# Kernel optimization log

Hardware: AMD Instinct MI355X
Metric: run time of the kernel (lower is better)

## Reference

```python
import jax, jax.numpy as jnp
import numpy as np

B = 131072      # batch of states
N_ACT = 40      # output_dim (Tetris action space)


def setup_inputs() -> dict:
    key = jax.random.key(0)
    ks = jax.random.split(key, 9)
    # state vector: 11 real-valued board features, 1 hold-piece id in [0,4),
    # 3 next-piece ids in [1,8) (0 is treated as invalid by the original code)
    keep = jax.random.normal(ks[0], (B, 11), dtype=jnp.float32)
    hold = jax.random.randint(ks[1], (B, 1), 0, 4).astype(jnp.float32)
    nxt = jax.random.randint(ks[2], (B, 3), 1, 8).astype(jnp.float32)
    x = jnp.concatenate([keep, hold, nxt], axis=1)  # [B, 15]
    W1 = jax.random.normal(ks[3], (36, 128), dtype=jnp.float32) * 0.1
    b1 = jnp.zeros((128,), dtype=jnp.float32)
    W2 = jax.random.normal(ks[4], (128, 512), dtype=jnp.float32) * 0.05
    b2 = jnp.zeros((512,), dtype=jnp.float32)
    W4 = jax.random.normal(ks[5], (512, N_ACT), dtype=jnp.float32) * 0.05
    b4 = jnp.zeros((N_ACT,), dtype=jnp.float32)
    return {"x": x, "W1": W1, "b1": b1, "W2": W2, "b2": b2, "W4": W4, "b4": b4}


def reference(x, W1, b1, W2, b2, W4, b4):
    B_, _ = x.shape
    keep = x[:, :11]                                      # [B, 11]
    # vectorized replacement of the per-sample .item() one-hot loop
    hold_idx = jax.lax.stop_gradient(jnp.clip(x[:, 11].astype(jnp.int32), 0, 3))
    nxt_idx = jax.lax.stop_gradient(jnp.clip(x[:, 12:15].astype(jnp.int32) - 1, 0, 6))
    hold_oh = jax.nn.one_hot(hold_idx, 4, dtype=x.dtype)  # [B, 4]
    nxt_oh = jax.nn.one_hot(nxt_idx, 7, dtype=x.dtype).reshape(B_, 21)  # [B, 21]
    inp = jnp.concatenate([keep, hold_oh, nxt_oh], axis=1)  # [B, 36]
    h = jax.nn.relu(inp @ W1 + b1)   # [B, 128]
    h = jax.nn.relu(h @ W2 + b2)     # [B, 512]
    return h @ W4 + b4               # [B, N_ACT]
```

## Files before the change

### kernel.cpp

```cpp
#include <hip/hip_runtime.h>


typedef short bf16x8 __attribute__((ext_vector_type(8)));
typedef float f32x4 __attribute__((ext_vector_type(4)));
typedef unsigned int u32;

#define NW1F 8192
#define NW2F 65536
#define NW4F 24576
#define PACK_TOTAL (NW1F + NW2F + NW4F)
#define PACK_THREADS (PACK_TOTAL / 8)

#define SROW 72

__device__ __forceinline__ unsigned short f2bf(float f) {
  union { float f; unsigned u; } a; a.f = f;
  unsigned r = a.u + 0x7fffu + ((a.u >> 16) & 1u);
  return (unsigned short)(r >> 16);
}
__device__ __forceinline__ u32 cvtpk(float lo, float hi) {
  u32 r;
  asm("v_cvt_pk_bf16_f32 %0, %1, %2" : "=v"(r) : "v"(lo), "v"(hi));
  return r;
}

__global__ void pack_weights(const float* __restrict__ W1,
                             const float* __restrict__ W2,
                             const float* __restrict__ W4,
                             unsigned short* __restrict__ wf) {
  int t = blockIdx.x * 256 + threadIdx.x;
  if (t >= PACK_THREADS) return;
  int fid = t >> 6, lane = t & 63;
  int l16 = lane & 15, quad = lane >> 4;
  float vals[8];
  if (fid < 16) {
    int mt = fid >> 1, ks = fid & 1;
    int m = mt * 16 + l16, k0 = ks * 32 + quad * 8;
#pragma unroll
    for (int j = 0; j < 8; ++j) { int k = k0 + j; vals[j] = (k < 36) ? W1[k * 128 + m] : 0.f; }
  } else if (fid < 144) {
    int f = fid - 16, mt = f >> 2, ks = f & 3;
    int m = mt * 16 + l16, k0 = ks * 32 + quad * 8;
#pragma unroll
    for (int j = 0; j < 8; ++j) vals[j] = W2[(k0 + j) * 512 + m];
  } else {
    int f = fid - 144, mt = f >> 4, ks = f & 15;
    int m = mt * 16 + l16, k0 = ks * 32 + quad * 8;
#pragma unroll
    for (int j = 0; j < 8; ++j) vals[j] = (m < 40) ? W4[(k0 + j) * 40 + m] : 0.f;
  }
  u32 p[4];
#pragma unroll
  for (int j = 0; j < 4; ++j) p[j] = cvtpk(vals[2 * j], vals[2 * j + 1]);
  *(bf16x8*)(wf + (size_t)t * 8) = *(bf16x8*)p;
}

#define MTL_STEP(chunk, mtl)                                                   \
  {                                                                            \
    f32x4 bias2 = *(const f32x4*)(b2 + (chunk) * 64 + (mtl) * 16 + quad * 4);  \
    int fb = (chunk) * 16 + (mtl) * 4 + 4;                                     \
    if (fb >= 128) fb = 0;           \
    _Pragma("unroll")                                                          \
    for (int k = 0; k < 4; ++k)                                                \
      W[((mtl) + 1) & 1][k] = *(const bf16x8*)(w2p + (size_t)(fb + k) * 512);  \
    f32x4 acc2[2];                                                             \
    __builtin_amdgcn_s_setprio(1);                                             \
    _Pragma("unroll")                                                          \
    for (int rg = 0; rg < 2; ++rg)                                             \
      acc2[rg] = __builtin_amdgcn_mfma_f32_16x16x32_bf16(                      \
          W[(mtl) & 1][0], af1[rg][0], bias2, 0, 0, 0);                        \
    _Pragma("unroll")                                                          \
    for (int ks = 1; ks < 4; ++ks)                                             \
      _Pragma("unroll")                                                        \
      for (int rg = 0; rg < 2; ++rg)                                           \
        acc2[rg] = __builtin_amdgcn_mfma_f32_16x16x32_bf16(                    \
            W[(mtl) & 1][ks], af1[rg][ks], acc2[rg], 0, 0, 0);                 \
    __builtin_amdgcn_s_setprio(0);                                             \
    _Pragma("unroll")                                                          \
    for (int rg = 0; rg < 2; ++rg) {                                           \
      float v0 = fmaxf(acc2[rg][0], 0.f);                                      \
      float v1 = fmaxf(acc2[rg][1], 0.f);                                      \
      float v2 = fmaxf(acc2[rg][2], 0.f);                                      \
      float v3 = fmaxf(acc2[rg][3], 0.f);                                      \
      uint2 pk = {cvtpk(v0, v1), cvtpk(v2, v3)};                               \
      *(uint2*)(su + (rg * 16 + l16) * SROW + (mtl) * 16 + quad * 4) = pk;     \
    }                                                                          \
  }

#define H_READ(dst, ks3)                                                       \
  _Pragma("unroll")                                                            \
  for (int rg = 0; rg < 2; ++rg)                                               \
    dst[rg] = *(const bf16x8*)(su + (rg * 16 + l16) * SROW + (ks3) * 32 + quad * 8);

#define W4_LOAD(dst, chunkprev, ks3)                                           \
  _Pragma("unroll")                                                            \
  for (int mt3 = 0; mt3 < 3; ++mt3)                                            \
    dst[mt3] = *(const bf16x8*)(                                               \
        w4f + (size_t)((mt3 * 16 + (chunkprev) * 2 + (ks3)) * 64 + lane) * 8);

#define L3_PART(w4q, hq)                                                       \
  __builtin_amdgcn_s_setprio(1);                                               \
  _Pragma("unroll")                                                            \
  for (int mt3 = 0; mt3 < 3; ++mt3)                                            \
    _Pragma("unroll")                                                          \
    for (int rg = 0; rg < 2; ++rg)                                             \
      accO[mt3][rg] = __builtin_amdgcn_mfma_f32_16x16x32_bf16(                 \
          w4q[mt3], hq[rg], accO[mt3][rg], 0, 0, 0);                           \
  __builtin_amdgcn_s_setprio(0);

__global__ __launch_bounds__(128, 4) void dqn_fused(
    const float* __restrict__ x,
    const unsigned short* __restrict__ wf,
    const float* __restrict__ b1,
    const float* __restrict__ b2,
    const float* __restrict__ b4,
    float* __restrict__ out) {
  __shared__ __align__(16) unsigned short sBuf[2 * 32 * SROW];

  const int tid  = threadIdx.x;
  const int lane = tid & 63;
  const int wave = tid >> 6;
  const int quad = lane >> 4;
  const int l16  = lane & 15;
  const int row0 = blockIdx.x << 6;
  const int lr0  = wave * 32;
  unsigned short* su = sBuf + wave * (32 * SROW);

  const unsigned short* w2f = wf + NW1F;
  const unsigned short* w4f = wf + NW1F + NW2F;
  const unsigned short* w2p = w2f + lane * 8;

  bf16x8 W[2][4];
#pragma unroll
  for (int k = 0; k < 4; ++k) W[0][k] = *(const bf16x8*)(w2p + (size_t)k * 512);

  if (lane < 32) {
    const float* xr = x + (size_t)(row0 + lr0 + lane) * 15;
    unsigned short* dst = su + lane * SROW;
    bf16x8 z = {0, 0, 0, 0, 0, 0, 0, 0};
#pragma unroll
    for (int c = 8; c < 64; c += 8) *(bf16x8*)(dst + c) = z;
    u32 p[4];
#pragma unroll
    for (int i = 0; i < 4; ++i) p[i] = cvtpk(xr[2 * i], xr[2 * i + 1]);
    *(bf16x8*)dst = *(bf16x8*)p;
    *(u32*)(dst + 8) = cvtpk(xr[8], xr[9]);
    dst[10] = f2bf(xr[10]);
    int hold = (int)xr[11]; hold = hold < 0 ? 0 : (hold > 3 ? 3 : hold);
    dst[11 + hold] = 0x3F80;
#pragma unroll
    for (int t = 0; t < 3; ++t) {
      int nx = (int)xr[12 + t] - 1; nx = nx < 0 ? 0 : (nx > 6 ? 6 : nx);
      dst[15 + t * 7 + nx] = 0x3F80;
    }
  }

  const f32x4 vzero = {0.f, 0.f, 0.f, 0.f};

  bf16x8 ib[2][2];
#pragma unroll
  for (int rg = 0; rg < 2; ++rg)
#pragma unroll
    for (int ks = 0; ks < 2; ++ks)
      ib[rg][ks] = *(const bf16x8*)(su + (rg * 16 + l16) * SROW + ks * 32 + quad * 8);

  bf16x8 af1[2][4];
#pragma unroll
  for (int half = 0; half < 2; ++half) {
    bf16x8 wa[4][2];
#pragma unroll
    for (int mtl = 0; mtl < 4; ++mtl)
#pragma unroll
      for (int ks = 0; ks < 2; ++ks)
        wa[mtl][ks] = *(const bf16x8*)(
            wf + (size_t)(((half * 4 + mtl) * 2 + ks) * 64 + lane) * 8);

#pragma unroll
    for (int mtl = 0; mtl < 4; ++mtl) {
      f32x4 bias1 = *(const f32x4*)(b1 + (half * 4 + mtl) * 16 + quad * 4);
      f32x4 acc1[2];
      __builtin_amdgcn_s_setprio(1);
#pragma unroll
      for (int rg = 0; rg < 2; ++rg)
        acc1[rg] = __builtin_amdgcn_mfma_f32_16x16x32_bf16(wa[mtl][0], ib[rg][0], bias1, 0, 0, 0);
#pragma unroll
      for (int rg = 0; rg < 2; ++rg)
        acc1[rg] = __builtin_amdgcn_mfma_f32_16x16x32_bf16(wa[mtl][1], ib[rg][1], acc1[rg], 0, 0, 0);
      __builtin_amdgcn_s_setprio(0);
#pragma unroll
      for (int rg = 0; rg < 2; ++rg) {
        float v0 = fmaxf(acc1[rg][0], 0.f);
        float v1 = fmaxf(acc1[rg][1], 0.f);
        float v2 = fmaxf(acc1[rg][2], 0.f);
        float v3 = fmaxf(acc1[rg][3], 0.f);
        uint2 pk = {cvtpk(v0, v1), cvtpk(v2, v3)};
        *(uint2*)(su + (rg * 16 + l16) * SROW + mtl * 16 + quad * 4) = pk;
      }
    }
#pragma unroll
    for (int rg = 0; rg < 2; ++rg)
#pragma unroll
      for (int ksl = 0; ksl < 2; ++ksl)
        af1[rg][half * 2 + ksl] =
            *(const bf16x8*)(su + (rg * 16 + l16) * SROW + ksl * 32 + quad * 8);
  }

  f32x4 accO[3][2];
#pragma unroll
  for (int mt = 0; mt < 3; ++mt)
#pragma unroll
    for (int rg = 0; rg < 2; ++rg) accO[mt][rg] = vzero;

  MTL_STEP(0, 0)
  MTL_STEP(0, 1)
  MTL_STEP(0, 2)
  MTL_STEP(0, 3)
  for (int chunk = 1; chunk < 8; ++chunk) {
    bf16x8 h0[2];
    H_READ(h0, 0)
    MTL_STEP(chunk, 0)
    MTL_STEP(chunk, 1)
    bf16x8 w4a[3];
    W4_LOAD(w4a, chunk - 1, 0)
    L3_PART(w4a, h0)
    bf16x8 h1v[2];
    H_READ(h1v, 1)
    MTL_STEP(chunk, 2)
    MTL_STEP(chunk, 3)
    bf16x8 w4b[3];
    W4_LOAD(w4b, chunk - 1, 1)
    L3_PART(w4b, h1v)
  }
  {
    bf16x8 h0[2];
    H_READ(h0, 0)
    bf16x8 h1v[2];
    H_READ(h1v, 1)
    bf16x8 w4a[3];
    W4_LOAD(w4a, 7, 0)
    L3_PART(w4a, h0)
    bf16x8 w4b[3];
    W4_LOAD(w4b, 7, 1)
    L3_PART(w4b, h1v)
  }

#pragma unroll
  for (int mt3 = 0; mt3 < 3; ++mt3) {
    int colbase = mt3 * 16 + quad * 4;
    if (colbase < 40) {
      f32x4 bias = *(const f32x4*)(b4 + colbase);
#pragma unroll
      for (int rg = 0; rg < 2; ++rg) {
        f32x4 v = accO[mt3][rg] + bias;
        size_t row = (size_t)(row0 + lr0 + rg * 16 + l16);
        *(f32x4*)(out + row * 40 + colbase) = v;
      }
    }
  }
}

extern "C" void kernel_launch(void* const* d_in, const int* in_sizes, int n_in,
                              void* d_out, int out_size, void* d_ws, size_t ws_size,
                              hipStream_t stream) {
  const float* x  = (const float*)d_in[0];
  const float* W1 = (const float*)d_in[1];
  const float* b1 = (const float*)d_in[2];
  const float* W2 = (const float*)d_in[3];
  const float* b2 = (const float*)d_in[4];
  const float* W4 = (const float*)d_in[5];
  const float* b4 = (const float*)d_in[6];
  float* out = (float*)d_out;
  unsigned short* wf = (unsigned short*)d_ws;

  int B = in_sizes[0] / 15;

  hipLaunchKernelGGL(pack_weights, dim3((PACK_THREADS + 255) / 256), dim3(256), 0, stream,
                     W1, W2, W4, wf);
  hipLaunchKernelGGL(dqn_fused, dim3(B / 64), dim3(128), 0, stream,
                     x, wf, b1, b2, b4, out);
}
```

Baseline: 111.4 us.

## Fold hold one-hot into bias, shrink layer-1 K, double rows per wave

The hold-piece one-hot is folded into a per-hold bias table (b1 plus the matching W1 row), precomputed in the pack kernel. This cuts layer-1 K from 36 to 32, so it needs one MFMA k-step instead of two. Each wave now processes 64 rows instead of 32, building its input fragments directly in registers from x instead of staging them through LDS. That reuses every loaded W2/W4 fragment across twice as many rows. Launch bounds drop to 2 blocks, setprio hints are removed and the chunk loop is fully unrolled, at the cost of higher register pressure and half as many blocks.

```diff
diff --git a/kernel.cpp b/kernel.cpp
--- a/kernel.cpp
+++ b/kernel.cpp
@@ -5,7 +5,7 @@
 typedef float f32x4 __attribute__((ext_vector_type(4)));
 typedef unsigned int u32;
 
-#define NW1F 8192
+#define NW1F 4096
 #define NW2F 65536
 #define NW4F 24576
 #define PACK_TOTAL (NW1F + NW2F + NW4F)
@@ -13,11 +13,6 @@
 
 #define SROW 72
 
-__device__ __forceinline__ unsigned short f2bf(float f) {
-  union { float f; unsigned u; } a; a.f = f;
-  unsigned r = a.u + 0x7fffu + ((a.u >> 16) & 1u);
-  return (unsigned short)(r >> 16);
-}
 __device__ __forceinline__ u32 cvtpk(float lo, float hi) {
   u32 r;
   asm("v_cvt_pk_bf16_f32 %0, %1, %2" : "=v"(r) : "v"(lo), "v"(hi));
@@ -25,26 +20,38 @@
 }
 
 __global__ void pack_weights(const float* __restrict__ W1,
+                             const float* __restrict__ b1,
                              const float* __restrict__ W2,
                              const float* __restrict__ W4,
                              unsigned short* __restrict__ wf) {
   int t = blockIdx.x * 256 + threadIdx.x;
-  if (t >= PACK_THREADS) return;
+  if (t >= PACK_THREADS) {
+    int f = t - PACK_THREADS;
+    if (f < 128) {
+      float* bh = (float*)(wf + PACK_TOTAL);
+#pragma unroll
+      for (int h = 0; h < 4; ++h) bh[h * 128 + f] = b1[f] + W1[(11 + h) * 128 + f];
+    }
+    return;
+  }
   int fid = t >> 6, lane = t & 63;
   int l16 = lane & 15, quad = lane >> 4;
   float vals[8];
-  if (fid < 16) {
-    int mt = fid >> 1, ks = fid & 1;
-    int m = mt * 16 + l16, k0 = ks * 32 + quad * 8;
-#pragma unroll
-    for (int j = 0; j < 8; ++j) { int k = k0 + j; vals[j] = (k < 36) ? W1[k * 128 + m] : 0.f; }
-  } else if (fid < 144) {
-    int f = fid - 16, mt = f >> 2, ks = f & 3;
+  if (fid < 8) {
+    int m = fid * 16 + l16, k0 = quad * 8;
+#pragma unroll
+    for (int j = 0; j < 8; ++j) {
+      int k = k0 + j;
+      int orig = (k < 11) ? k : k + 4;
+      vals[j] = W1[orig * 128 + m];
+    }
+  } else if (fid < 136) {
+    int f = fid - 8, mt = f >> 2, ks = f & 3;
     int m = mt * 16 + l16, k0 = ks * 32 + quad * 8;
 #pragma unroll
     for (int j = 0; j < 8; ++j) vals[j] = W2[(k0 + j) * 512 + m];
   } else {
-    int f = fid - 144, mt = f >> 4, ks = f & 15;
+    int f = fid - 136, mt = f >> 4, ks = f & 15;
     int m = mt * 16 + l16, k0 = ks * 32 + quad * 8;
 #pragma unroll
     for (int j = 0; j < 8; ++j) vals[j] = (m < 40) ? W4[(k0 + j) * 40 + m] : 0.f;
@@ -57,27 +64,24 @@
 
 #define MTL_STEP(chunk, mtl)                                                   \
   {                                                                            \
-    f32x4 bias2 = *(const f32x4*)(b2 + (chunk) * 64 + (mtl) * 16 + quad * 4);  \
-    int fb = (chunk) * 16 + (mtl) * 4 + 4;                                     \
-    if (fb >= 128) fb = 0;           \
+    const int fb = ((chunk) * 16 + (mtl) * 4 + 4) & 127;                       \
     _Pragma("unroll")                                                          \
     for (int k = 0; k < 4; ++k)                                                \
       W[((mtl) + 1) & 1][k] = *(const bf16x8*)(w2p + (size_t)(fb + k) * 512);  \
-    f32x4 acc2[2];                                                             \
-    __builtin_amdgcn_s_setprio(1);                                             \
-    _Pragma("unroll")                                                          \
-    for (int rg = 0; rg < 2; ++rg)                                             \
+    f32x4 bias2 = *(const f32x4*)(b2 + (chunk) * 64 + (mtl) * 16 + quad * 4);  \
+    f32x4 acc2[4];                                                             \
+    _Pragma("unroll")                                                          \
+    for (int rg = 0; rg < 4; ++rg)                                             \
       acc2[rg] = __builtin_amdgcn_mfma_f32_16x16x32_bf16(                      \
           W[(mtl) & 1][0], af1[rg][0], bias2, 0, 0, 0);                        \
     _Pragma("unroll")                                                          \
     for (int ks = 1; ks < 4; ++ks)                                             \
       _Pragma("unroll")                                                        \
-      for (int rg = 0; rg < 2; ++rg)                                           \
+      for (int rg = 0; rg < 4; ++rg)                                           \
         acc2[rg] = __builtin_amdgcn_mfma_f32_16x16x32_bf16(                    \
             W[(mtl) & 1][ks], af1[rg][ks], acc2[rg], 0, 0, 0);                 \
-    __builtin_amdgcn_s_setprio(0);                                             \
-    _Pragma("unroll")                                                          \
-    for (int rg = 0; rg < 2; ++rg) {                                           \
+    _Pragma("unroll")                                                          \
+    for (int rg = 0; rg < 4; ++rg) {                                           \
       float v0 = fmaxf(acc2[rg][0], 0.f);                                      \
       float v1 = fmaxf(acc2[rg][1], 0.f);                                      \
       float v2 = fmaxf(acc2[rg][2], 0.f);                                      \
@@ -89,7 +93,7 @@
 
 #define H_READ(dst, ks3)                                                       \
   _Pragma("unroll")                                                            \
-  for (int rg = 0; rg < 2; ++rg)                                               \
+  for (int rg = 0; rg < 4; ++rg)                                               \
     dst[rg] = *(const bf16x8*)(su + (rg * 16 + l16) * SROW + (ks3) * 32 + quad * 8);
 
 #define W4_LOAD(dst, chunkprev, ks3)                                           \
@@ -99,96 +103,114 @@
         w4f + (size_t)((mt3 * 16 + (chunkprev) * 2 + (ks3)) * 64 + lane) * 8);
 
 #define L3_PART(w4q, hq)                                                       \
-  __builtin_amdgcn_s_setprio(1);                                               \
   _Pragma("unroll")                                                            \
   for (int mt3 = 0; mt3 < 3; ++mt3)                                            \
     _Pragma("unroll")                                                          \
-    for (int rg = 0; rg < 2; ++rg)                                             \
+    for (int rg = 0; rg < 4; ++rg)                                             \
       accO[mt3][rg] = __builtin_amdgcn_mfma_f32_16x16x32_bf16(                 \
-          w4q[mt3], hq[rg], accO[mt3][rg], 0, 0, 0);                           \
-  __builtin_amdgcn_s_setprio(0);
-
-__global__ __launch_bounds__(128, 4) void dqn_fused(
+          w4q[mt3], hq[rg], accO[mt3][rg], 0, 0, 0);
+
+#define CHUNK_BODY(c)                                                          \
+  {                                                                            \
+    bf16x8 h0[4], h1v[4], w4a[3], w4b[3];                                      \
+    H_READ(h0, 0)                                                              \
+    W4_LOAD(w4a, (c) - 1, 0)                                                   \
+    MTL_STEP(c, 0)                                                             \
+    MTL_STEP(c, 1)                                                             \
+    L3_PART(w4a, h0)                                                           \
+    H_READ(h1v, 1)                                                             \
+    W4_LOAD(w4b, (c) - 1, 1)                                                   \
+    MTL_STEP(c, 2)                                                             \
+    MTL_STEP(c, 3)                                                             \
+    L3_PART(w4b, h1v)                                                          \
+  }
+
+__global__ __launch_bounds__(128, 2) void dqn_fused(
     const float* __restrict__ x,
     const unsigned short* __restrict__ wf,
-    const float* __restrict__ b1,
     const float* __restrict__ b2,
     const float* __restrict__ b4,
     float* __restrict__ out) {
-  __shared__ __align__(16) unsigned short sBuf[2 * 32 * SROW];
+  __shared__ __align__(16) unsigned short sBuf[2 * 64 * SROW];
 
   const int tid  = threadIdx.x;
   const int lane = tid & 63;
   const int wave = tid >> 6;
   const int quad = lane >> 4;
   const int l16  = lane & 15;
-  const int row0 = blockIdx.x << 6;
-  const int lr0  = wave * 32;
-  unsigned short* su = sBuf + wave * (32 * SROW);
+  const int row0 = blockIdx.x << 7;
+  const int lr0  = wave * 64;
+  unsigned short* su = sBuf + wave * (64 * SROW);
 
   const unsigned short* w2f = wf + NW1F;
   const unsigned short* w4f = wf + NW1F + NW2F;
+  const float* b1h = (const float*)(wf + PACK_TOTAL);
   const unsigned short* w2p = w2f + lane * 8;
 
   bf16x8 W[2][4];
 #pragma unroll
   for (int k = 0; k < 4; ++k) W[0][k] = *(const bf16x8*)(w2p + (size_t)k * 512);
 
-  if (lane < 32) {
-    const float* xr = x + (size_t)(row0 + lr0 + lane) * 15;
-    unsigned short* dst = su + lane * SROW;
-    bf16x8 z = {0, 0, 0, 0, 0, 0, 0, 0};
-#pragma unroll
-    for (int c = 8; c < 64; c += 8) *(bf16x8*)(dst + c) = z;
-    u32 p[4];
-#pragma unroll
-    for (int i = 0; i < 4; ++i) p[i] = cvtpk(xr[2 * i], xr[2 * i + 1]);
-    *(bf16x8*)dst = *(bf16x8*)p;
-    *(u32*)(dst + 8) = cvtpk(xr[8], xr[9]);
-    dst[10] = f2bf(xr[10]);
-    int hold = (int)xr[11]; hold = hold < 0 ? 0 : (hold > 3 ? 3 : hold);
-    dst[11 + hold] = 0x3F80;
-#pragma unroll
-    for (int t = 0; t < 3; ++t) {
-      int nx = (int)xr[12 + t] - 1; nx = nx < 0 ? 0 : (nx > 6 ? 6 : nx);
-      dst[15 + t * 7 + nx] = 0x3F80;
-    }
-  }
-
-  const f32x4 vzero = {0.f, 0.f, 0.f, 0.f};
-
-  bf16x8 ib[2][2];
-#pragma unroll
-  for (int rg = 0; rg < 2; ++rg)
-#pragma unroll
-    for (int ks = 0; ks < 2; ++ks)
-      ib[rg][ks] = *(const bf16x8*)(su + (rg * 16 + l16) * SROW + ks * 32 + quad * 8);
-
-  bf16x8 af1[2][4];
+  bf16x8 ib[4];
+  int hold[4];
+#pragma unroll
+  for (int rg = 0; rg < 4; ++rg) {
+    const float* xr = x + (size_t)(row0 + lr0 + rg * 16 + l16) * 15;
+    float a0 = xr[0], a1 = xr[1], a2 = xr[2], a3 = xr[3];
+    float b0 = xr[4], b1v = xr[5], b2v = xr[6], b3 = xr[7];
+    float c0 = xr[8], c1 = xr[9], c2 = xr[10], c3 = xr[11];
+    float d0 = xr[12], d1 = xr[13], d2 = xr[14];
+    int hd = (int)c3; hd = hd < 0 ? 0 : (hd > 3 ? 3 : hd); hold[rg] = hd;
+    int n0 = (int)d0 - 1; n0 = n0 < 0 ? 0 : (n0 > 6 ? 6 : n0);
+    int n1 = (int)d1 - 1; n1 = n1 < 0 ? 0 : (n1 > 6 ? 6 : n1);
+    int n2 = (int)d2 - 1; n2 = n2 < 0 ? 0 : (n2 > 6 ? 6 : n2);
+    u32 w0, w1, w2, w3;
+    if (quad == 0) {
+      w0 = cvtpk(a0, a1); w1 = cvtpk(a2, a3);
+      w2 = cvtpk(b0, b1v); w3 = cvtpk(b2v, b3);
+    } else if (quad == 1) {
+      w0 = cvtpk(c0, c1);
+      w1 = cvtpk(c2, n0 == 0 ? 1.f : 0.f);
+      w2 = cvtpk(n0 == 1 ? 1.f : 0.f, n0 == 2 ? 1.f : 0.f);
+      w3 = cvtpk(n0 == 3 ? 1.f : 0.f, n0 == 4 ? 1.f : 0.f);
+    } else if (quad == 2) {
+      w0 = cvtpk(n0 == 5 ? 1.f : 0.f, n0 == 6 ? 1.f : 0.f);
+      w1 = cvtpk(n1 == 0 ? 1.f : 0.f, n1 == 1 ? 1.f : 0.f);
+      w2 = cvtpk(n1 == 2 ? 1.f : 0.f, n1 == 3 ? 1.f : 0.f);
+      w3 = cvtpk(n1 == 4 ? 1.f : 0.f, n1 == 5 ? 1.f : 0.f);
+    } else {
+      w0 = cvtpk(n1 == 6 ? 1.f : 0.f, n2 == 0 ? 1.f : 0.f);
+      w1 = cvtpk(n2 == 1 ? 1.f : 0.f, n2 == 2 ? 1.f : 0.f);
+      w2 = cvtpk(n2 == 3 ? 1.f : 0.f, n2 == 4 ? 1.f : 0.f);
+      w3 = cvtpk(n2 == 5 ? 1.f : 0.f, n2 == 6 ? 1.f : 0.f);
+    }
+    u32 ww[4] = {w0, w1, w2, w3};
+    ib[rg] = *(bf16x8*)ww;
+  }
+
+  bf16x8 af1[4][4];
 #pragma unroll
   for (int half = 0; half < 2; ++half) {
-    bf16x8 wa[4][2];
+    bf16x8 wa[4];
 #pragma unroll
     for (int mtl = 0; mtl < 4; ++mtl)
-#pragma unroll
-      for (int ks = 0; ks < 2; ++ks)
-        wa[mtl][ks] = *(const bf16x8*)(
-            wf + (size_t)(((half * 4 + mtl) * 2 + ks) * 64 + lane) * 8);
+      wa[mtl] = *(const bf16x8*)(wf + (size_t)((half * 4 + mtl) * 64 + lane) * 8);
+    f32x4 cB[4][4];
+#pragma unroll
+    for (int mtl = 0; mtl < 4; ++mtl)
+#pragma unroll
+      for (int rg = 0; rg < 4; ++rg)
+        cB[mtl][rg] = *(const f32x4*)(
+            b1h + hold[rg] * 128 + (half * 4 + mtl) * 16 + quad * 4);
 
 #pragma unroll
     for (int mtl = 0; mtl < 4; ++mtl) {
-      f32x4 bias1 = *(const f32x4*)(b1 + (half * 4 + mtl) * 16 + quad * 4);
-      f32x4 acc1[2];
-      __builtin_amdgcn_s_setprio(1);
-#pragma unroll
-      for (int rg = 0; rg < 2; ++rg)
-        acc1[rg] = __builtin_amdgcn_mfma_f32_16x16x32_bf16(wa[mtl][0], ib[rg][0], bias1, 0, 0, 0);
-#pragma unroll
-      for (int rg = 0; rg < 2; ++rg)
-        acc1[rg] = __builtin_amdgcn_mfma_f32_16x16x32_bf16(wa[mtl][1], ib[rg][1], acc1[rg], 0, 0, 0);
-      __builtin_amdgcn_s_setprio(0);
-#pragma unroll
-      for (int rg = 0; rg < 2; ++rg) {
+      f32x4 acc1[4];
+#pragma unroll
+      for (int rg = 0; rg < 4; ++rg)
+        acc1[rg] = __builtin_amdgcn_mfma_f32_16x16x32_bf16(wa[mtl], ib[rg], cB[mtl][rg], 0, 0, 0);
+#pragma unroll
+      for (int rg = 0; rg < 4; ++rg) {
         float v0 = fmaxf(acc1[rg][0], 0.f);
         float v1 = fmaxf(acc1[rg][1], 0.f);
         float v2 = fmaxf(acc1[rg][2], 0.f);
@@ -198,49 +220,38 @@
       }
     }
 #pragma unroll
-    for (int rg = 0; rg < 2; ++rg)
+    for (int rg = 0; rg < 4; ++rg)
 #pragma unroll
       for (int ksl = 0; ksl < 2; ++ksl)
         af1[rg][half * 2 + ksl] =
             *(const bf16x8*)(su + (rg * 16 + l16) * SROW + ksl * 32 + quad * 8);
   }
 
-  f32x4 accO[3][2];
+  const f32x4 vzero = {0.f, 0.f, 0.f, 0.f};
+  f32x4 accO[3][4];
 #pragma unroll
   for (int mt = 0; mt < 3; ++mt)
 #pragma unroll
-    for (int rg = 0; rg < 2; ++rg) accO[mt][rg] = vzero;
+    for (int rg = 0; rg < 4; ++rg) accO[mt][rg] = vzero;
 
   MTL_STEP(0, 0)
   MTL_STEP(0, 1)
   MTL_STEP(0, 2)
   MTL_STEP(0, 3)
-  for (int chunk = 1; chunk < 8; ++chunk) {
-    bf16x8 h0[2];
+  CHUNK_BODY(1)
+  CHUNK_BODY(2)
+  CHUNK_BODY(3)
+  CHUNK_BODY(4)
+  CHUNK_BODY(5)
+  CHUNK_BODY(6)
+  CHUNK_BODY(7)
+  {
+    bf16x8 h0[4], h1v[4], w4a[3], w4b[3];
     H_READ(h0, 0)
-    MTL_STEP(chunk, 0)
-    MTL_STEP(chunk, 1)
-    bf16x8 w4a[3];
-    W4_LOAD(w4a, chunk - 1, 0)
+    H_READ(h1v, 1)
+    W4_LOAD(w4a, 7, 0)
+    W4_LOAD(w4b, 7, 1)
     L3_PART(w4a, h0)
-    bf16x8 h1v[2];
-    H_READ(h1v, 1)
-    MTL_STEP(chunk, 2)
-    MTL_STEP(chunk, 3)
-    bf16x8 w4b[3];
-    W4_LOAD(w4b, chunk - 1, 1)
-    L3_PART(w4b, h1v)
-  }
-  {
-    bf16x8 h0[2];
-    H_READ(h0, 0)
-    bf16x8 h1v[2];
-    H_READ(h1v, 1)
-    bf16x8 w4a[3];
-    W4_LOAD(w4a, 7, 0)
-    L3_PART(w4a, h0)
-    bf16x8 w4b[3];
-    W4_LOAD(w4b, 7, 1)
     L3_PART(w4b, h1v)
   }
 
@@ -250,7 +261,7 @@
     if (colbase < 40) {
       f32x4 bias = *(const f32x4*)(b4 + colbase);
 #pragma unroll
-      for (int rg = 0; rg < 2; ++rg) {
+      for (int rg = 0; rg < 4; ++rg) {
         f32x4 v = accO[mt3][rg] + bias;
         size_t row = (size_t)(row0 + lr0 + rg * 16 + l16);
         *(f32x4*)(out + row * 40 + colbase) = v;
@@ -274,8 +285,8 @@
 
   int B = in_sizes[0] / 15;
 
-  hipLaunchKernelGGL(pack_weights, dim3((PACK_THREADS + 255) / 256), dim3(256), 0, stream,
-                     W1, W2, W4, wf);
-  hipLaunchKernelGGL(dqn_fused, dim3(B / 64), dim3(128), 0, stream,
-                     x, wf, b1, b2, b4, out);
-}
+  hipLaunchKernelGGL(pack_weights, dim3((PACK_THREADS + 128 + 255) / 256), dim3(256), 0, stream,
+                     W1, b1, W2, W4, wf);
+  hipLaunchKernelGGL(dqn_fused, dim3(B / 128), dim3(128), 0, stream,
+                     x, wf, b2, b4, out);
+}
```

Result: faster. 104.4 us (-6.3%).
